# Kernel optimization log

Measured on AMD Instinct MI355X. Metric: run time of the kernel, lower is better.

The kernel has to match this reference:

```python
import jax, jax.numpy as jnp
import numpy as np

TOP_K = 2
NUM_EXPERTS = 8


def setup_inputs() -> dict:
    key = jax.random.key(0)
    ks = jax.random.split(key, 5)
    d_model, d_ff, E = 1024, 2048, NUM_EXPERTS
    B, S = 4, 1024
    scale = 1.0 / np.sqrt(d_model)
    return {
        "x": jax.random.normal(ks[0], (B, S, d_model), jnp.float32),
        "gate_w": jax.random.normal(ks[1], (E, d_model), jnp.float32) * scale,
        "w1": jax.random.normal(ks[2], (E, d_ff, d_model), jnp.float32) * scale,
        "w3": jax.random.normal(ks[3], (E, d_ff, d_model), jnp.float32) * scale,
        "w2": jax.random.normal(ks[4], (E, d_model, d_ff), jnp.float32) * (1.0 / np.sqrt(d_ff)),
    }


def reference(x, gate_w, w1, w3, w2):
    B, S, d = x.shape
    E = gate_w.shape[0]
    T = B * S

    # Router (eval mode: no noise)
    router_logits = jnp.einsum("bsd,ed->bse", x, gate_w)  # (B,S,E)
    top_logits, top_idx = jax.lax.top_k(router_logits, TOP_K)  # (B,S,k)
    routing_weights = jax.nn.softmax(top_logits, axis=-1)

    x_flat = x.reshape(T, d)
    idx_flat = top_idx.reshape(T, TOP_K)
    rw_flat = routing_weights.reshape(T, TOP_K)

    # (T,E) combine weights: topk indices are distinct, so one-hot sum is exact
    one_hot = jax.nn.one_hot(idx_flat, E, dtype=x.dtype)  # (T,k,E)
    combine = jnp.einsum("tke,tk->te", one_hot, rw_flat)  # (T,E)

    # Dense grouped SwiGLU: run every expert over all tokens, weight-combine.
    h = jnp.einsum("td,efd->tef", x_flat, w1)  # (T,E,d_ff)
    v = jnp.einsum("td,efd->tef", x_flat, w3)
    y = jax.nn.silu(h) * v
    expert_out = jnp.einsum("tef,edf->ted", y, w2)  # (T,E,d)
    out_flat = jnp.einsum("ted,te->td", expert_out, combine)
    output = out_flat.reshape(B, S, d)

    # Auxiliary load-balance loss
    router_probs = jax.nn.softmax(router_logits, axis=-1)  # (B,S,E)
    expert_probs = router_probs.mean(axis=(0, 1))  # (E,)
    counts = one_hot.sum(axis=(0, 1))  # (E,)
    expert_fraction = counts / (T * TOP_K)
    aux_loss = jnp.sum(expert_probs * expert_fraction) * E

    return output, aux_loss
```

## Files before the change

### kernel.cpp

```cpp
#include <hip/hip_runtime.h>
#include <hip/hip_bf16.h>
#include <stdint.h>

#define T_TOK 4096
#define DM    1024
#define DF    2048
#define NE    8
#define RROWS 8192
#define BM    128
#define BK    64
#define MAXT  72

typedef __attribute__((ext_vector_type(8))) short bf16x8;
typedef __attribute__((ext_vector_type(4))) float f32x4;

static __device__ __forceinline__ unsigned short f2bf(float f) {
  union { float f; unsigned u; } v; v.f = f;
  unsigned r = v.u + 0x7fffu + ((v.u >> 16) & 1u);
  return (unsigned short)(r >> 16);
}

static __device__ __forceinline__ void glds16(const void* g, void* l) {
  __builtin_amdgcn_global_load_lds(
      (__attribute__((address_space(1))) void*)(g),
      (__attribute__((address_space(3))) void*)(l), 16, 0, 0);
}

__global__ __launch_bounds__(256) void cvt_kernel(const float* __restrict__ src,
                                                  unsigned short* __restrict__ dst, int n4) {
  int stride = gridDim.x * blockDim.x;
  for (int i = blockIdx.x * blockDim.x + threadIdx.x; i < n4; i += stride) {
    float4 f = ((const float4*)src)[i];
    ushort4 u;
    u.x = f2bf(f.x); u.y = f2bf(f.y); u.z = f2bf(f.z); u.w = f2bf(f.w);
    ((ushort4*)dst)[i] = u;
  }
}

__global__ __launch_bounds__(256) void router_kernel(
    const float* __restrict__ x, const float* __restrict__ gw,
    unsigned short* __restrict__ xb,
    int* __restrict__ topk_idx, float* __restrict__ topk_w,
    int* __restrict__ pc, float* __restrict__ pp) {
  __shared__ int lc[8];
  __shared__ float lp[8];
  int wave = threadIdx.x >> 6;
  int lane = threadIdx.x & 63;
  if (threadIdx.x < 8) { lc[threadIdx.x] = 0; lp[threadIdx.x] = 0.f; }
  __syncthreads();

  int t = blockIdx.x * 4 + wave;

  const float4* xp = (const float4*)(x + (size_t)t * DM);
  float4 xv[4];
#pragma unroll
  for (int q = 0; q < 4; ++q) xv[q] = xp[lane + 64 * q];

  ushort4* xbp = (ushort4*)(xb + (size_t)t * DM);
#pragma unroll
  for (int q = 0; q < 4; ++q) {
    ushort4 u;
    u.x = f2bf(xv[q].x); u.y = f2bf(xv[q].y); u.z = f2bf(xv[q].z); u.w = f2bf(xv[q].w);
    xbp[lane + 64 * q] = u;
  }

  float l[NE];
#pragma unroll
  for (int e = 0; e < NE; ++e) {
    const float4* gp = (const float4*)(gw + (size_t)e * DM);
    float s = 0.f;
#pragma unroll
    for (int q = 0; q < 4; ++q) {
      float4 g4 = gp[lane + 64 * q];
      s += xv[q].x * g4.x + xv[q].y * g4.y + xv[q].z * g4.z + xv[q].w * g4.w;
    }
#pragma unroll
    for (int off = 32; off > 0; off >>= 1) s += __shfl_xor(s, off);
    l[e] = s;
  }

  float m = l[0];
#pragma unroll
  for (int e = 1; e < NE; ++e) m = fmaxf(m, l[e]);
  float p[NE], ps = 0.f;
#pragma unroll
  for (int e = 0; e < NE; ++e) { p[e] = expf(l[e] - m); ps += p[e]; }

  int i1 = 0; float v1 = l[0];
#pragma unroll
  for (int e = 1; e < NE; ++e) if (l[e] > v1) { v1 = l[e]; i1 = e; }
  int i2 = -1; float v2 = -1e30f;
#pragma unroll
  for (int e = 0; e < NE; ++e) if (e != i1 && l[e] > v2) { v2 = l[e]; i2 = e; }

  float r2 = expf(v2 - v1);
  float inv12 = 1.f / (1.f + r2);

  if (lane == 0) {
    topk_idx[t * 2] = i1; topk_idx[t * 2 + 1] = i2;
    topk_w[t * 2] = inv12; topk_w[t * 2 + 1] = r2 * inv12;
    atomicAdd(&lc[i1], 1);
    atomicAdd(&lc[i2], 1);
    float inv = 1.f / ps;
#pragma unroll
    for (int e = 0; e < NE; ++e) atomicAdd(&lp[e], p[e] * inv);
  }
  __syncthreads();
  if (threadIdx.x < 8) {
    pc[blockIdx.x * 8 + threadIdx.x] = lc[threadIdx.x];
    pp[blockIdx.x * 8 + threadIdx.x] = lp[threadIdx.x];
  }
}

__global__ __launch_bounds__(512) void reduce_aux_kernel(
    const int* __restrict__ pc, const float* __restrict__ pp,
    int* __restrict__ counts, float* __restrict__ out_aux) {
  __shared__ int sc[8];
  __shared__ float sp[8];
  int wave = threadIdx.x >> 6;
  int lane = threadIdx.x & 63;
  int c = 0; float p = 0.f;
#pragma unroll
  for (int j = 0; j < 16; ++j) {
    int idx = lane + 64 * j;
    c += pc[idx * 8 + wave];
    p += pp[idx * 8 + wave];
  }
#pragma unroll
  for (int off = 32; off > 0; off >>= 1) {
    c += __shfl_xor(c, off);
    p += __shfl_xor(p, off);
  }
  if (lane == 0) { sc[wave] = c; sp[wave] = p; counts[wave] = c; }
  __syncthreads();
  if (threadIdx.x == 0) {
    float s = 0.f;
#pragma unroll
    for (int e = 0; e < NE; ++e)
      s += (sp[e] / (float)T_TOK) * ((float)sc[e] / (float)(T_TOK * 2));
    *out_aux = s * (float)NE;
  }
}

__global__ void build_tiles_kernel(const int* __restrict__ counts, int* __restrict__ offsets,
                                   int* __restrict__ tiledesc, int* __restrict__ ntiles) {
  if (threadIdx.x != 0 || blockIdx.x != 0) return;
  int off = 0, nt = 0;
  for (int e = 0; e < NE; ++e) {
    offsets[e] = off;
    int n = counts[e];
    for (int r0 = 0; r0 < n; r0 += BM) {
      int rem = n - r0;
      tiledesc[nt * 3 + 0] = e;
      tiledesc[nt * 3 + 1] = off + r0;
      tiledesc[nt * 3 + 2] = rem < BM ? rem : BM;
      ++nt;
    }
    off += n;
  }
  offsets[NE] = off;
  *ntiles = nt;
}

__global__ __launch_bounds__(256) void scatter_kernel(
    const int* __restrict__ topk_idx, const float* __restrict__ topk_w,
    const int* __restrict__ offsets, int* __restrict__ fill,
    int* __restrict__ btok, float* __restrict__ bw) {
  __shared__ int lcnt[8], lbase[8];
  int i = blockIdx.x * 256 + threadIdx.x;
  if (threadIdx.x < 8) lcnt[threadIdx.x] = 0;
  __syncthreads();
  int e = topk_idx[i];
  int pos = atomicAdd(&lcnt[e], 1);
  __syncthreads();
  if (threadIdx.x < 8) lbase[threadIdx.x] = atomicAdd(&fill[threadIdx.x], lcnt[threadIdx.x]);
  __syncthreads();
  int j = offsets[e] + lbase[e] + pos;
  btok[j] = i >> 1;
  bw[j] = topk_w[i];
}

template <bool WB16>
__global__ __launch_bounds__(512) void gemm1_kernel(
    const unsigned short* __restrict__ xb,
    const void* __restrict__ w1p, const void* __restrict__ w3p,
    unsigned short* __restrict__ Y,
    const int* __restrict__ btok,
    const int* __restrict__ tiledesc, const int* __restrict__ ntiles) {
  int flat = blockIdx.y * MAXT + blockIdx.x;
  int total = MAXT * (DF / 128);
  int nid = (flat & 7) * (total >> 3) + (flat >> 3);
  int mt = nid % MAXT;
  int fb = nid / MAXT;

  if (mt >= *ntiles) return;
  int e    = tiledesc[mt * 3 + 0];
  int row0 = tiledesc[mt * 3 + 1];
  int mcnt = tiledesc[mt * 3 + 2];
  int f0   = fb * 128;

  __shared__ __align__(16) unsigned short sA[128 * 64];
  __shared__ __align__(16) unsigned short sB1[128 * 64];
  __shared__ __align__(16) unsigned short sB3[128 * 64];

  int tid = threadIdx.x;
  int w = tid >> 6, lane = tid & 63;
  int wm = w >> 2, wn = w & 3;

  int rA0 = w * 8 + (lane >> 3);
  int rA1 = rA0 + 64;
  int colb = (((lane & 7) ^ (lane >> 3)) << 4);
  int tok0 = btok[row0 + ((rA0 < mcnt) ? rA0 : 0)];
  int tok1 = btok[row0 + ((rA1 < mcnt) ? rA1 : 0)];

  const char* xbc = (const char*)xb;
  const char* w1c = (const char*)w1p;
  const char* w3c = (const char*)w3p;

  f32x4 acch[4][2] = {};
  f32x4 accv[4][2] = {};

  for (int k0 = 0; k0 < DM; k0 += BK) {
    __syncthreads();
    glds16(xbc + (((size_t)tok0 * DM + k0) * 2) + colb, (char*)sA + w * 1024);
    glds16(xbc + (((size_t)tok1 * DM + k0) * 2) + colb, (char*)sA + (w + 8) * 1024);
    if constexpr (WB16) {
      glds16(w1c + (((size_t)(e * DF + f0 + rA0) * DM + k0) * 2) + colb, (char*)sB1 + w * 1024);
      glds16(w1c + (((size_t)(e * DF + f0 + rA1) * DM + k0) * 2) + colb, (char*)sB1 + (w + 8) * 1024);
      glds16(w3c + (((size_t)(e * DF + f0 + rA0) * DM + k0) * 2) + colb, (char*)sB3 + w * 1024);
      glds16(w3c + (((size_t)(e * DF + f0 + rA1) * DM + k0) * 2) + colb, (char*)sB3 + (w + 8) * 1024);
    } else {
#pragma unroll
      for (int it = 0; it < 4; ++it) {
        int gidx = tid + it * 512;
        int r = gidx >> 4;
        int cb8 = (gidx & 15) * 8;
        int sw = cb8 ^ ((r & 7) << 4);
        size_t gbyte = (((size_t)(e * DF + f0 + r) * DM + k0) * 4) + (size_t)cb8 * 2;
        float4 f1 = *(const float4*)(w1c + gbyte);
        float4 f3 = *(const float4*)(w3c + gbyte);
        ushort4 u1, u3;
        u1.x = f2bf(f1.x); u1.y = f2bf(f1.y); u1.z = f2bf(f1.z); u1.w = f2bf(f1.w);
        u3.x = f2bf(f3.x); u3.y = f2bf(f3.y); u3.z = f2bf(f3.z); u3.w = f2bf(f3.w);
        *(ushort4*)((char*)sB1 + r * 128 + sw) = u1;
        *(ushort4*)((char*)sB3 + r * 128 + sw) = u3;
      }
    }
    __syncthreads();

#pragma unroll
    for (int kk = 0; kk < 2; ++kk) {
      int kb = ((lane >> 4) << 4) + kk * 64;
      bf16x8 a[4], b1f[2], b3f[2];
#pragma unroll
      for (int m = 0; m < 4; ++m) {
        int r = wm * 64 + m * 16 + (lane & 15);
        a[m] = *(const bf16x8*)((const char*)sA + r * 128 + (kb ^ ((r & 7) << 4)));
      }
#pragma unroll
      for (int n = 0; n < 2; ++n) {
        int rf = wn * 32 + n * 16 + (lane & 15);
        int ob = rf * 128 + (kb ^ ((rf & 7) << 4));
        b1f[n] = *(const bf16x8*)((const char*)sB1 + ob);
        b3f[n] = *(const bf16x8*)((const char*)sB3 + ob);
      }
#pragma unroll
      for (int m = 0; m < 4; ++m)
#pragma unroll
        for (int n = 0; n < 2; ++n) {
          acch[m][n] = __builtin_amdgcn_mfma_f32_16x16x32_bf16(a[m], b1f[n], acch[m][n], 0, 0, 0);
          accv[m][n] = __builtin_amdgcn_mfma_f32_16x16x32_bf16(a[m], b3f[n], accv[m][n], 0, 0, 0);
        }
    }
  }

#pragma unroll
  for (int m = 0; m < 4; ++m) {
#pragma unroll
    for (int j = 0; j < 4; ++j) {
      int rl = wm * 64 + m * 16 + (lane >> 4) * 4 + j;
      if (rl < mcnt) {
        size_t yrow = (size_t)(row0 + rl) * DF + f0;
#pragma unroll
        for (int n = 0; n < 2; ++n) {
          float h = acch[m][n][j], v = accv[m][n][j];
          float y = (h / (1.f + expf(-h))) * v;
          Y[yrow + wn * 32 + n * 16 + (lane & 15)] = f2bf(y);
        }
      }
    }
  }
}

template <bool WB16>
__global__ __launch_bounds__(512) void gemm2_kernel(
    const unsigned short* __restrict__ Y,
    const void* __restrict__ w2p,
    float* __restrict__ out,
    const int* __restrict__ btok, const float* __restrict__ bw,
    const int* __restrict__ tiledesc, const int* __restrict__ ntiles) {
  int flat = blockIdx.y * MAXT + blockIdx.x;
  int total = MAXT * (DM / 128);
  int nid = (flat & 7) * (total >> 3) + (flat >> 3);
  int mt = nid % MAXT;
  int cb = nid / MAXT;

  if (mt >= *ntiles) return;
  int e    = tiledesc[mt * 3 + 0];
  int row0 = tiledesc[mt * 3 + 1];
  int mcnt = tiledesc[mt * 3 + 2];
  int c0   = cb * 128;

  __shared__ __align__(16) unsigned short sA[128 * 64];
  __shared__ __align__(16) unsigned short sB[128 * 64];

  int tid = threadIdx.x;
  int w = tid >> 6, lane = tid & 63;
  int wm = w >> 2, wn = w & 3;

  int rA0 = w * 8 + (lane >> 3);
  int rA1 = rA0 + 64;
  int colb = (((lane & 7) ^ (lane >> 3)) << 4);

  const char* yc  = (const char*)Y;
  const char* w2c = (const char*)w2p;

  f32x4 acc[4][2] = {};

  for (int k0 = 0; k0 < DF; k0 += BK) {
    __syncthreads();
    glds16(yc + (((size_t)(row0 + rA0) * DF + k0) * 2) + colb, (char*)sA + w * 1024);
    glds16(yc + (((size_t)(row0 + rA1) * DF + k0) * 2) + colb, (char*)sA + (w + 8) * 1024);
    if constexpr (WB16) {
      glds16(w2c + (((size_t)(e * DM + c0 + rA0) * DF + k0) * 2) + colb, (char*)sB + w * 1024);
      glds16(w2c + (((size_t)(e * DM + c0 + rA1) * DF + k0) * 2) + colb, (char*)sB + (w + 8) * 1024);
    } else {
#pragma unroll
      for (int it = 0; it < 4; ++it) {
        int gidx = tid + it * 512;
        int r = gidx >> 4;
        int cb8 = (gidx & 15) * 8;
        int sw = cb8 ^ ((r & 7) << 4);
        size_t gbyte = (((size_t)(e * DM + c0 + r) * DF + k0) * 4) + (size_t)cb8 * 2;
        float4 f = *(const float4*)(w2c + gbyte);
        ushort4 u;
        u.x = f2bf(f.x); u.y = f2bf(f.y); u.z = f2bf(f.z); u.w = f2bf(f.w);
        *(ushort4*)((char*)sB + r * 128 + sw) = u;
      }
    }
    __syncthreads();

#pragma unroll
    for (int kk = 0; kk < 2; ++kk) {
      int kb = ((lane >> 4) << 4) + kk * 64;
      bf16x8 a[4], b[2];
#pragma unroll
      for (int m = 0; m < 4; ++m) {
        int r = wm * 64 + m * 16 + (lane & 15);
        a[m] = *(const bf16x8*)((const char*)sA + r * 128 + (kb ^ ((r & 7) << 4)));
      }
#pragma unroll
      for (int n = 0; n < 2; ++n) {
        int rf = wn * 32 + n * 16 + (lane & 15);
        b[n] = *(const bf16x8*)((const char*)sB + rf * 128 + (kb ^ ((rf & 7) << 4)));
      }
#pragma unroll
      for (int m = 0; m < 4; ++m)
#pragma unroll
        for (int n = 0; n < 2; ++n)
          acc[m][n] = __builtin_amdgcn_mfma_f32_16x16x32_bf16(a[m], b[n], acc[m][n], 0, 0, 0);
    }
  }

#pragma unroll
  for (int m = 0; m < 4; ++m) {
#pragma unroll
    for (int j = 0; j < 4; ++j) {
      int rl = wm * 64 + m * 16 + (lane >> 4) * 4 + j;
      if (rl < mcnt) {
        int tok = btok[row0 + rl];
        float wgt = bw[row0 + rl];
#pragma unroll
        for (int n = 0; n < 2; ++n) {
          int col = c0 + wn * 32 + n * 16 + (lane & 15);
          atomicAdd(&out[(size_t)tok * DM + col], wgt * acc[m][n][j]);
        }
      }
    }
  }
}

extern "C" void kernel_launch(void* const* d_in, const int* in_sizes, int n_in,
                              void* d_out, int out_size, void* d_ws, size_t ws_size,
                              hipStream_t stream) {
  const float* x  = (const float*)d_in[0];
  const float* gw = (const float*)d_in[1];
  const float* w1 = (const float*)d_in[2];
  const float* w3 = (const float*)d_in[3];
  const float* w2 = (const float*)d_in[4];
  float* out = (float*)d_out;

  char* ws = (char*)d_ws;
  size_t o = 0;
  auto alloc = [&](size_t b) { size_t r = o; o = (o + b + 255) & ~(size_t)255; return r; };
  size_t o_tidx = alloc((size_t)RROWS * 4);
  size_t o_tw   = alloc((size_t)RROWS * 4);
  size_t o_meta = alloc(4096);
  size_t o_desc = alloc((size_t)MAXT * 3 * 4);
  size_t o_btok = alloc((size_t)RROWS * 4);
  size_t o_bw   = alloc((size_t)RROWS * 4);
  size_t o_pc   = alloc((size_t)1024 * 8 * 4);
  size_t o_pp   = alloc((size_t)1024 * 8 * 4);
  size_t o_xb   = alloc((size_t)T_TOK * DM * 2);
  size_t o_Y    = alloc((size_t)(RROWS + 128) * DF * 2);
  size_t o_w1b  = alloc((size_t)NE * DF * DM * 2);
  size_t o_w3b  = alloc((size_t)NE * DF * DM * 2);
  size_t o_w2b  = alloc((size_t)NE * DM * DF * 2);
  size_t need_full = o;
  bool full = ws_size >= need_full;

  int* tidx   = (int*)(ws + o_tidx);
  float* tw   = (float*)(ws + o_tw);
  int* meta   = (int*)(ws + o_meta);
  int* counts = meta;
  int* fill   = meta + 8;
  int* offs   = meta + 16;
  int* ntiles = meta + 25;
  int* desc   = (int*)(ws + o_desc);
  int* btok   = (int*)(ws + o_btok);
  float* bw   = (float*)(ws + o_bw);
  int* pc     = (int*)(ws + o_pc);
  float* pp   = (float*)(ws + o_pp);
  unsigned short* xb = (unsigned short*)(ws + o_xb);
  unsigned short* Y  = (unsigned short*)(ws + o_Y);

  hipMemsetAsync(ws + o_meta, 0, 256, stream);
  hipMemsetAsync(d_out, 0, (size_t)T_TOK * DM * 4, stream);

  if (full) {
    cvt_kernel<<<2048, 256, 0, stream>>>(w1, (unsigned short*)(ws + o_w1b), NE * DF * DM / 4);
    cvt_kernel<<<2048, 256, 0, stream>>>(w3, (unsigned short*)(ws + o_w3b), NE * DF * DM / 4);
    cvt_kernel<<<2048, 256, 0, stream>>>(w2, (unsigned short*)(ws + o_w2b), NE * DM * DF / 4);
  }

  router_kernel<<<T_TOK / 4, 256, 0, stream>>>(x, gw, xb, tidx, tw, pc, pp);
  reduce_aux_kernel<<<1, 512, 0, stream>>>(pc, pp, counts, out + (size_t)T_TOK * DM);
  build_tiles_kernel<<<1, 1, 0, stream>>>(counts, offs, desc, ntiles);
  scatter_kernel<<<RROWS / 256, 256, 0, stream>>>(tidx, tw, offs, fill, btok, bw);

  if (full) {
    gemm1_kernel<true><<<dim3(MAXT, DF / 128), 512, 0, stream>>>(
        xb, ws + o_w1b, ws + o_w3b, Y, btok, desc, ntiles);
    gemm2_kernel<true><<<dim3(MAXT, DM / 128), 512, 0, stream>>>(
        Y, ws + o_w2b, out, btok, bw, desc, ntiles);
  } else {
    gemm1_kernel<false><<<dim3(MAXT, DF / 128), 512, 0, stream>>>(
        xb, w1, w3, Y, btok, desc, ntiles);
    gemm2_kernel<false><<<dim3(MAXT, DM / 128), 512, 0, stream>>>(
        Y, w2, out, btok, bw, desc, ntiles);
  }
}
```

Before: 264.6 us.

## Double M tile to 256, double-buffer LDS in expert GEMMs, merge weight casts

Both expert GEMMs now use 256-row token tiles (MAXT drops to 40), and each wave computes a 64x64 sub-tile instead of 64x32. This raises data reuse per shared-memory load and halves the redundant weight traffic across M tiles. The K loop is double-buffered: the next stage's async global-to-LDS loads are issued before the current stage's MFMAs, so memory latency overlaps compute. The three fp32→bf16 weight conversion launches are merged into one kernel with a 3-row grid. In exchange, LDS use and register pressure both rise, which likely limits occupancy to one block per CU.

After: 320.9 us. +21.3%, slower.

```diff
diff --git a/kernel.cpp b/kernel.cpp
--- a/kernel.cpp
+++ b/kernel.cpp
@@ -7,9 +7,9 @@
 #define DF    2048
 #define NE    8
 #define RROWS 8192
-#define BM    128
+#define BM    256
 #define BK    64
-#define MAXT  72
+#define MAXT  40
 
 typedef __attribute__((ext_vector_type(8))) short bf16x8;
 typedef __attribute__((ext_vector_type(4))) float f32x4;
@@ -26,8 +26,12 @@
       (__attribute__((address_space(3))) void*)(l), 16, 0, 0);
 }
 
-__global__ __launch_bounds__(256) void cvt_kernel(const float* __restrict__ src,
-                                                  unsigned short* __restrict__ dst, int n4) {
+__global__ __launch_bounds__(256) void cvt3_kernel(
+    const float* __restrict__ w1, const float* __restrict__ w3, const float* __restrict__ w2,
+    unsigned short* __restrict__ d1, unsigned short* __restrict__ d3, unsigned short* __restrict__ d2,
+    int n4) {
+  const float* src = blockIdx.y == 0 ? w1 : (blockIdx.y == 1 ? w3 : w2);
+  unsigned short* dst = blockIdx.y == 0 ? d1 : (blockIdx.y == 1 ? d3 : d2);
   int stride = gridDim.x * blockDim.x;
   for (int i = blockIdx.x * blockDim.x + threadIdx.x; i < n4; i += stride) {
     float4 f = ((const float4*)src)[i];
@@ -181,14 +185,14 @@
 }
 
 template <bool WB16>
-__global__ __launch_bounds__(512) void gemm1_kernel(
+__global__ __launch_bounds__(512, 2) void gemm1_kernel(
     const unsigned short* __restrict__ xb,
     const void* __restrict__ w1p, const void* __restrict__ w3p,
     unsigned short* __restrict__ Y,
     const int* __restrict__ btok,
     const int* __restrict__ tiledesc, const int* __restrict__ ntiles) {
   int flat = blockIdx.y * MAXT + blockIdx.x;
-  int total = MAXT * (DF / 128);
+  const int total = MAXT * (DF / 128);
   int nid = (flat & 7) * (total >> 3) + (flat >> 3);
   int mt = nid % MAXT;
   int fb = nid / MAXT;
@@ -199,36 +203,42 @@
   int mcnt = tiledesc[mt * 3 + 2];
   int f0   = fb * 128;
 
-  __shared__ __align__(16) unsigned short sA[128 * 64];
-  __shared__ __align__(16) unsigned short sB1[128 * 64];
-  __shared__ __align__(16) unsigned short sB3[128 * 64];
+  __shared__ __align__(16) unsigned short sA[2][BM * BK];
+  __shared__ __align__(16) unsigned short sB1[2][128 * BK];
+  __shared__ __align__(16) unsigned short sB3[2][128 * BK];
 
   int tid = threadIdx.x;
   int w = tid >> 6, lane = tid & 63;
-  int wm = w >> 2, wn = w & 3;
-
-  int rA0 = w * 8 + (lane >> 3);
-  int rA1 = rA0 + 64;
+  int wm = w >> 1, wn = w & 1;
   int colb = (((lane & 7) ^ (lane >> 3)) << 4);
-  int tok0 = btok[row0 + ((rA0 < mcnt) ? rA0 : 0)];
-  int tok1 = btok[row0 + ((rA1 < mcnt) ? rA1 : 0)];
+  int srow = w * 8 + (lane >> 3);
+
+  int tokr[4];
+#pragma unroll
+  for (int r = 0; r < 4; ++r) {
+    int row = r * 64 + srow;
+    tokr[r] = btok[row0 + ((row < mcnt) ? row : 0)];
+  }
 
   const char* xbc = (const char*)xb;
   const char* w1c = (const char*)w1p;
   const char* w3c = (const char*)w3p;
 
-  f32x4 acch[4][2] = {};
-  f32x4 accv[4][2] = {};
-
-  for (int k0 = 0; k0 < DM; k0 += BK) {
-    __syncthreads();
-    glds16(xbc + (((size_t)tok0 * DM + k0) * 2) + colb, (char*)sA + w * 1024);
-    glds16(xbc + (((size_t)tok1 * DM + k0) * 2) + colb, (char*)sA + (w + 8) * 1024);
+  f32x4 acch[4][4] = {};
+  f32x4 accv[4][4] = {};
+
+  auto stage = [&](int k0, int buf) {
+#pragma unroll
+    for (int r = 0; r < 4; ++r)
+      glds16(xbc + ((size_t)tokr[r] * DM + k0) * 2 + colb,
+             (char*)sA[buf] + r * 8192 + w * 1024);
     if constexpr (WB16) {
-      glds16(w1c + (((size_t)(e * DF + f0 + rA0) * DM + k0) * 2) + colb, (char*)sB1 + w * 1024);
-      glds16(w1c + (((size_t)(e * DF + f0 + rA1) * DM + k0) * 2) + colb, (char*)sB1 + (w + 8) * 1024);
-      glds16(w3c + (((size_t)(e * DF + f0 + rA0) * DM + k0) * 2) + colb, (char*)sB3 + w * 1024);
-      glds16(w3c + (((size_t)(e * DF + f0 + rA1) * DM + k0) * 2) + colb, (char*)sB3 + (w + 8) * 1024);
+#pragma unroll
+      for (int r = 0; r < 2; ++r) {
+        size_t broff = ((size_t)(e * DF + f0 + r * 64 + srow) * DM + k0) * 2;
+        glds16(w1c + broff + colb, (char*)sB1[buf] + r * 8192 + w * 1024);
+        glds16(w3c + broff + colb, (char*)sB3[buf] + r * 8192 + w * 1024);
+      }
     } else {
 #pragma unroll
       for (int it = 0; it < 4; ++it) {
@@ -236,42 +246,50 @@
         int r = gidx >> 4;
         int cb8 = (gidx & 15) * 8;
         int sw = cb8 ^ ((r & 7) << 4);
-        size_t gbyte = (((size_t)(e * DF + f0 + r) * DM + k0) * 4) + (size_t)cb8 * 2;
+        size_t gbyte = ((size_t)(e * DF + f0 + r) * DM + k0) * 4 + (size_t)cb8 * 2;
         float4 f1 = *(const float4*)(w1c + gbyte);
         float4 f3 = *(const float4*)(w3c + gbyte);
         ushort4 u1, u3;
         u1.x = f2bf(f1.x); u1.y = f2bf(f1.y); u1.z = f2bf(f1.z); u1.w = f2bf(f1.w);
         u3.x = f2bf(f3.x); u3.y = f2bf(f3.y); u3.z = f2bf(f3.z); u3.w = f2bf(f3.w);
-        *(ushort4*)((char*)sB1 + r * 128 + sw) = u1;
-        *(ushort4*)((char*)sB3 + r * 128 + sw) = u3;
-      }
-    }
-    __syncthreads();
-
+        *(ushort4*)((char*)sB1[buf] + r * 128 + sw) = u1;
+        *(ushort4*)((char*)sB3[buf] + r * 128 + sw) = u3;
+      }
+    }
+  };
+
+  stage(0, 0);
+  __syncthreads();
+  int cur = 0;
+  const int NT = DM / BK;
+  for (int t = 0; t < NT; ++t) {
+    if (t < NT - 1) stage((t + 1) * BK, cur ^ 1);
 #pragma unroll
     for (int kk = 0; kk < 2; ++kk) {
       int kb = ((lane >> 4) << 4) + kk * 64;
-      bf16x8 a[4], b1f[2], b3f[2];
+      bf16x8 a[4], b1[4], b3[4];
 #pragma unroll
       for (int m = 0; m < 4; ++m) {
         int r = wm * 64 + m * 16 + (lane & 15);
-        a[m] = *(const bf16x8*)((const char*)sA + r * 128 + (kb ^ ((r & 7) << 4)));
-      }
-#pragma unroll
-      for (int n = 0; n < 2; ++n) {
-        int rf = wn * 32 + n * 16 + (lane & 15);
+        a[m] = *(const bf16x8*)((const char*)sA[cur] + r * 128 + (kb ^ ((r & 7) << 4)));
+      }
+#pragma unroll
+      for (int n = 0; n < 4; ++n) {
+        int rf = wn * 64 + n * 16 + (lane & 15);
         int ob = rf * 128 + (kb ^ ((rf & 7) << 4));
-        b1f[n] = *(const bf16x8*)((const char*)sB1 + ob);
-        b3f[n] = *(const bf16x8*)((const char*)sB3 + ob);
+        b1[n] = *(const bf16x8*)((const char*)sB1[cur] + ob);
+        b3[n] = *(const bf16x8*)((const char*)sB3[cur] + ob);
       }
 #pragma unroll
       for (int m = 0; m < 4; ++m)
 #pragma unroll
-        for (int n = 0; n < 2; ++n) {
-          acch[m][n] = __builtin_amdgcn_mfma_f32_16x16x32_bf16(a[m], b1f[n], acch[m][n], 0, 0, 0);
-          accv[m][n] = __builtin_amdgcn_mfma_f32_16x16x32_bf16(a[m], b3f[n], accv[m][n], 0, 0, 0);
+        for (int n = 0; n < 4; ++n) {
+          acch[m][n] = __builtin_amdgcn_mfma_f32_16x16x32_bf16(a[m], b1[n], acch[m][n], 0, 0, 0);
+          accv[m][n] = __builtin_amdgcn_mfma_f32_16x16x32_bf16(a[m], b3[n], accv[m][n], 0, 0, 0);
         }
     }
+    __syncthreads();
+    cur ^= 1;
   }
 
 #pragma unroll
@@ -282,10 +300,10 @@
       if (rl < mcnt) {
         size_t yrow = (size_t)(row0 + rl) * DF + f0;
 #pragma unroll
-        for (int n = 0; n < 2; ++n) {
+        for (int n = 0; n < 4; ++n) {
           float h = acch[m][n][j], v = accv[m][n][j];
           float y = (h / (1.f + expf(-h))) * v;
-          Y[yrow + wn * 32 + n * 16 + (lane & 15)] = f2bf(y);
+          Y[yrow + wn * 64 + n * 16 + (lane & 15)] = f2bf(y);
         }
       }
     }
@@ -293,14 +311,14 @@
 }
 
 template <bool WB16>
-__global__ __launch_bounds__(512) void gemm2_kernel(
+__global__ __launch_bounds__(512, 2) void gemm2_kernel(
     const unsigned short* __restrict__ Y,
     const void* __restrict__ w2p,
     float* __restrict__ out,
     const int* __restrict__ btok, const float* __restrict__ bw,
     const int* __restrict__ tiledesc, const int* __restrict__ ntiles) {
   int flat = blockIdx.y * MAXT + blockIdx.x;
-  int total = MAXT * (DM / 128);
+  const int total = MAXT * (DM / 128);
   int nid = (flat & 7) * (total >> 3) + (flat >> 3);
   int mt = nid % MAXT;
   int cb = nid / MAXT;
@@ -311,29 +329,31 @@
   int mcnt = tiledesc[mt * 3 + 2];
   int c0   = cb * 128;
 
-  __shared__ __align__(16) unsigned short sA[128 * 64];
-  __shared__ __align__(16) unsigned short sB[128 * 64];
+  __shared__ __align__(16) unsigned short sA[2][BM * BK];
+  __shared__ __align__(16) unsigned short sB[2][128 * BK];
 
   int tid = threadIdx.x;
   int w = tid >> 6, lane = tid & 63;
-  int wm = w >> 2, wn = w & 3;
-
-  int rA0 = w * 8 + (lane >> 3);
-  int rA1 = rA0 + 64;
+  int wm = w >> 1, wn = w & 1;
   int colb = (((lane & 7) ^ (lane >> 3)) << 4);
+  int srow = w * 8 + (lane >> 3);
 
   const char* yc  = (const char*)Y;
   const char* w2c = (const char*)w2p;
 
-  f32x4 acc[4][2] = {};
-
-  for (int k0 = 0; k0 < DF; k0 += BK) {
-    __syncthreads();
-    glds16(yc + (((size_t)(row0 + rA0) * DF + k0) * 2) + colb, (char*)sA + w * 1024);
-    glds16(yc + (((size_t)(row0 + rA1) * DF + k0) * 2) + colb, (char*)sA + (w + 8) * 1024);
+  f32x4 acc[4][4] = {};
+
+  auto stage = [&](int k0, int buf) {
+#pragma unroll
+    for (int r = 0; r < 4; ++r)
+      glds16(yc + ((size_t)(row0 + r * 64 + srow) * DF + k0) * 2 + colb,
+             (char*)sA[buf] + r * 8192 + w * 1024);
     if constexpr (WB16) {
-      glds16(w2c + (((size_t)(e * DM + c0 + rA0) * DF + k0) * 2) + colb, (char*)sB + w * 1024);
-      glds16(w2c + (((size_t)(e * DM + c0 + rA1) * DF + k0) * 2) + colb, (char*)sB + (w + 8) * 1024);
+#pragma unroll
+      for (int r = 0; r < 2; ++r) {
+        size_t broff = ((size_t)(e * DM + c0 + r * 64 + srow) * DF + k0) * 2;
+        glds16(w2c + broff + colb, (char*)sB[buf] + r * 8192 + w * 1024);
+      }
     } else {
 #pragma unroll
       for (int it = 0; it < 4; ++it) {
@@ -341,35 +361,43 @@
         int r = gidx >> 4;
         int cb8 = (gidx & 15) * 8;
         int sw = cb8 ^ ((r & 7) << 4);
-        size_t gbyte = (((size_t)(e * DM + c0 + r) * DF + k0) * 4) + (size_t)cb8 * 2;
+        size_t gbyte = ((size_t)(e * DM + c0 + r) * DF + k0) * 4 + (size_t)cb8 * 2;
         float4 f = *(const float4*)(w2c + gbyte);
         ushort4 u;
         u.x = f2bf(f.x); u.y = f2bf(f.y); u.z = f2bf(f.z); u.w = f2bf(f.w);
-        *(ushort4*)((char*)sB + r * 128 + sw) = u;
-      }
-    }
-    __syncthreads();
-
+        *(ushort4*)((char*)sB[buf] + r * 128 + sw) = u;
+      }
+    }
+  };
+
+  stage(0, 0);
+  __syncthreads();
+  int cur = 0;
+  const int NT = DF / BK;
+  for (int t = 0; t < NT; ++t) {
+    if (t < NT - 1) stage((t + 1) * BK, cur ^ 1);
 #pragma unroll
     for (int kk = 0; kk < 2; ++kk) {
       int kb = ((lane >> 4) << 4) + kk * 64;
-      bf16x8 a[4], b[2];
+      bf16x8 a[4], b[4];
 #pragma unroll
       for (int m = 0; m < 4; ++m) {
         int r = wm * 64 + m * 16 + (lane & 15);
-        a[m] = *(const bf16x8*)((const char*)sA + r * 128 + (kb ^ ((r & 7) << 4)));
-      }
-#pragma unroll
-      for (int n = 0; n < 2; ++n) {
-        int rf = wn * 32 + n * 16 + (lane & 15);
-        b[n] = *(const bf16x8*)((const char*)sB + rf * 128 + (kb ^ ((rf & 7) << 4)));
+        a[m] = *(const bf16x8*)((const char*)sA[cur] + r * 128 + (kb ^ ((r & 7) << 4)));
+      }
+#pragma unroll
+      for (int n = 0; n < 4; ++n) {
+        int rf = wn * 64 + n * 16 + (lane & 15);
+        b[n] = *(const bf16x8*)((const char*)sB[cur] + rf * 128 + (kb ^ ((rf & 7) << 4)));
       }
 #pragma unroll
       for (int m = 0; m < 4; ++m)
 #pragma unroll
-        for (int n = 0; n < 2; ++n)
+        for (int n = 0; n < 4; ++n)
           acc[m][n] = __builtin_amdgcn_mfma_f32_16x16x32_bf16(a[m], b[n], acc[m][n], 0, 0, 0);
     }
+    __syncthreads();
+    cur ^= 1;
   }
 
 #pragma unroll
@@ -381,8 +409,8 @@
         int tok = btok[row0 + rl];
         float wgt = bw[row0 + rl];
 #pragma unroll
-        for (int n = 0; n < 2; ++n) {
-          int col = c0 + wn * 32 + n * 16 + (lane & 15);
+        for (int n = 0; n < 4; ++n) {
+          int col = c0 + wn * 64 + n * 16 + (lane & 15);
           atomicAdd(&out[(size_t)tok * DM + col], wgt * acc[m][n][j]);
         }
       }
@@ -412,7 +440,7 @@
   size_t o_pc   = alloc((size_t)1024 * 8 * 4);
   size_t o_pp   = alloc((size_t)1024 * 8 * 4);
   size_t o_xb   = alloc((size_t)T_TOK * DM * 2);
-  size_t o_Y    = alloc((size_t)(RROWS + 128) * DF * 2);
+  size_t o_Y    = alloc((size_t)(RROWS + 256) * DF * 2);
   size_t o_w1b  = alloc((size_t)NE * DF * DM * 2);
   size_t o_w3b  = alloc((size_t)NE * DF * DM * 2);
   size_t o_w2b  = alloc((size_t)NE * DM * DF * 2);
@@ -438,9 +466,10 @@
   hipMemsetAsync(d_out, 0, (size_t)T_TOK * DM * 4, stream);
 
   if (full) {
-    cvt_kernel<<<2048, 256, 0, stream>>>(w1, (unsigned short*)(ws + o_w1b), NE * DF * DM / 4);
-    cvt_kernel<<<2048, 256, 0, stream>>>(w3, (unsigned short*)(ws + o_w3b), NE * DF * DM / 4);
-    cvt_kernel<<<2048, 256, 0, stream>>>(w2, (unsigned short*)(ws + o_w2b), NE * DM * DF / 4);
+    cvt3_kernel<<<dim3(2048, 3), 256, 0, stream>>>(
+        w1, w3, w2,
+        (unsigned short*)(ws + o_w1b), (unsigned short*)(ws + o_w3b),
+        (unsigned short*)(ws + o_w2b), NE * DF * DM / 4);
   }
 
   router_kernel<<<T_TOK / 4, 256, 0, stream>>>(x, gw, xb, tidx, tw, pc, pp);
```

## Rewrite gate/up GEMM with 256-row tiles, double-buffered LDS and phased MFMA schedule

Applied to the files above, without the earlier changes.

Replaces the first grouped GEMM with a kernel that uses 256-row token tiles (a separate tile descriptor list), double-buffered shared memory, and an 8-phase schedule. The schedule interleaves async global-to-LDS prefetch of the next K step with MFMA clusters, using explicit vmcnt waits, barriers and setprio. The three weight-conversion launches are also merged into one 2D-grid kernel. Larger tiles raise weight reuse and the prefetch hides load latency. The cost is more registers and LDS per block, plus more padding waste on partial expert tiles.

Measured after the change: 273.3 us. 1.03x slower.

```diff
diff --git a/kernel.cpp b/kernel.cpp
--- a/kernel.cpp
+++ b/kernel.cpp
@@ -7,9 +7,9 @@
 #define DF    2048
 #define NE    8
 #define RROWS 8192
-#define BM    128
 #define BK    64
-#define MAXT  72
+#define MAXT1 40
+#define MAXT2 72
 
 typedef __attribute__((ext_vector_type(8))) short bf16x8;
 typedef __attribute__((ext_vector_type(4))) float f32x4;
@@ -26,8 +26,18 @@
       (__attribute__((address_space(3))) void*)(l), 16, 0, 0);
 }
 
-__global__ __launch_bounds__(256) void cvt_kernel(const float* __restrict__ src,
-                                                  unsigned short* __restrict__ dst, int n4) {
+#define VM_WAIT2 do { asm volatile("s_waitcnt vmcnt(2)" ::: "memory"); \
+                      __builtin_amdgcn_sched_barrier(0); } while (0)
+#define VM_WAIT0 do { asm volatile("s_waitcnt vmcnt(0)" ::: "memory"); \
+                      __builtin_amdgcn_sched_barrier(0); } while (0)
+#define BARRIER __builtin_amdgcn_s_barrier()
+
+__global__ __launch_bounds__(256) void cvt3_kernel(
+    const float* __restrict__ w1, const float* __restrict__ w3, const float* __restrict__ w2,
+    unsigned short* __restrict__ d1, unsigned short* __restrict__ d3, unsigned short* __restrict__ d2,
+    int n4) {
+  const float* src = blockIdx.y == 0 ? w1 : (blockIdx.y == 1 ? w3 : w2);
+  unsigned short* dst = blockIdx.y == 0 ? d1 : (blockIdx.y == 1 ? d3 : d2);
   int stride = gridDim.x * blockDim.x;
   for (int i = blockIdx.x * blockDim.x + threadIdx.x; i < n4; i += stride) {
     float4 f = ((const float4*)src)[i];
@@ -143,23 +153,28 @@
 }
 
 __global__ void build_tiles_kernel(const int* __restrict__ counts, int* __restrict__ offsets,
-                                   int* __restrict__ tiledesc, int* __restrict__ ntiles) {
+                                   int* __restrict__ d1, int* __restrict__ nt1p,
+                                   int* __restrict__ d2, int* __restrict__ nt2p) {
   if (threadIdx.x != 0 || blockIdx.x != 0) return;
-  int off = 0, nt = 0;
+  int off = 0, nt1 = 0, nt2 = 0;
   for (int e = 0; e < NE; ++e) {
     offsets[e] = off;
     int n = counts[e];
-    for (int r0 = 0; r0 < n; r0 += BM) {
+    for (int r0 = 0; r0 < n; r0 += 256) {
       int rem = n - r0;
-      tiledesc[nt * 3 + 0] = e;
-      tiledesc[nt * 3 + 1] = off + r0;
-      tiledesc[nt * 3 + 2] = rem < BM ? rem : BM;
-      ++nt;
+      d1[nt1 * 3 + 0] = e; d1[nt1 * 3 + 1] = off + r0; d1[nt1 * 3 + 2] = rem < 256 ? rem : 256;
+      ++nt1;
+    }
+    for (int r0 = 0; r0 < n; r0 += 128) {
+      int rem = n - r0;
+      d2[nt2 * 3 + 0] = e; d2[nt2 * 3 + 1] = off + r0; d2[nt2 * 3 + 2] = rem < 128 ? rem : 128;
+      ++nt2;
     }
     off += n;
   }
   offsets[NE] = off;
-  *ntiles = nt;
+  *nt1p = nt1;
+  *nt2p = nt2;
 }
 
 __global__ __launch_bounds__(256) void scatter_kernel(
@@ -180,19 +195,180 @@
   bw[j] = topk_w[i];
 }
 
-template <bool WB16>
-__global__ __launch_bounds__(512) void gemm1_kernel(
+__global__ __launch_bounds__(512, 2) void gemm1_8p(
     const unsigned short* __restrict__ xb,
-    const void* __restrict__ w1p, const void* __restrict__ w3p,
+    const unsigned short* __restrict__ w1b, const unsigned short* __restrict__ w3b,
+    unsigned short* __restrict__ Y,
+    const int* __restrict__ btok,
+    const int* __restrict__ desc1, const int* __restrict__ ntiles1) {
+  int flat = blockIdx.y * MAXT1 + blockIdx.x;
+  const int total = MAXT1 * (DF / 128);
+  int nid = (flat & 7) * (total >> 3) + (flat >> 3);
+  int mt = nid % MAXT1;
+  int fb = nid / MAXT1;
+  if (mt >= *ntiles1) return;
+  int e    = desc1[mt * 3 + 0];
+  int row0 = desc1[mt * 3 + 1];
+  int mcnt = desc1[mt * 3 + 2];
+  int f0   = fb * 128;
+
+  __shared__ __align__(16) unsigned short sA[2][256 * 64];
+  __shared__ __align__(16) unsigned short sB1[2][128 * 64];
+  __shared__ __align__(16) unsigned short sB3[2][128 * 64];
+
+  int tid = threadIdx.x;
+  int w = tid >> 6, lane = tid & 63;
+  int wm = w >> 2, wn = w & 3;
+  int sr = w * 8 + (lane >> 3);
+  int colb = ((lane & 7) ^ (lane >> 3)) << 4;
+  int kbase = (lane >> 4) * 16;
+
+  int tokr[4];
+#pragma unroll
+  for (int u = 0; u < 4; ++u) {
+    int row = u * 64 + sr;
+    tokr[u] = btok[row0 + ((row < mcnt) ? row : 0)];
+  }
+
+  const char* xc  = (const char*)xb;
+  const char* w1c = (const char*)w1b;
+  const char* w3c = (const char*)w3b;
+
+  f32x4 acch[8][2] = {};
+  f32x4 accv[8][2] = {};
+
+  auto stA = [&](int u, int k0, int b) {
+    glds16(xc + ((size_t)tokr[u] * DM + k0) * 2 + colb,
+           (char*)sA[b] + u * 8192 + w * 1024);
+  };
+  auto stB = [&](const char* wsrc, unsigned short* dst, int u, int k0) {
+    glds16(wsrc + ((size_t)(e * DF + f0 + u * 64 + sr) * DM + k0) * 2 + colb,
+           (char*)dst + u * 8192 + w * 1024);
+  };
+
+  stA(0, 0, 0); stA(1, 0, 0); stA(2, 0, 0); stA(3, 0, 0);
+  stB(w1c, sB1[0], 0, 0); stB(w1c, sB1[0], 1, 0);
+  stB(w3c, sB3[0], 0, 0); stB(w3c, sB3[0], 1, 0);
+  VM_WAIT2;
+  BARRIER;
+
+  const int NT = DM / BK;
+  int cur = 0;
+  for (int t = 0; t < NT; ++t) {
+    bool pre = (t + 1 < NT);
+    int k1 = (t + 1) * BK;
+    bf16x8 a0[8], a1[8], bf[2];
+
+#pragma unroll
+    for (int m = 0; m < 8; ++m) {
+      int r = wm * 128 + m * 16 + (lane & 15);
+      a0[m] = *(const bf16x8*)((const char*)sA[cur] + r * 128 + (kbase ^ ((r & 7) << 4)));
+    }
+#pragma unroll
+    for (int n = 0; n < 2; ++n) {
+      int r = n * 64 + wn * 16 + (lane & 15);
+      bf[n] = *(const bf16x8*)((const char*)sB1[cur] + r * 128 + (kbase ^ ((r & 7) << 4)));
+    }
+    if (pre) { stA(0, k1, cur ^ 1); stA(1, k1, cur ^ 1); VM_WAIT2; }
+    else VM_WAIT0;
+    BARRIER;
+    __builtin_amdgcn_s_setprio(1);
+#pragma unroll
+    for (int m = 0; m < 8; ++m)
+#pragma unroll
+      for (int n = 0; n < 2; ++n)
+        acch[m][n] = __builtin_amdgcn_mfma_f32_16x16x32_bf16(a0[m], bf[n], acch[m][n], 0, 0, 0);
+    __builtin_amdgcn_s_setprio(0);
+    BARRIER;
+
+#pragma unroll
+    for (int n = 0; n < 2; ++n) {
+      int r = n * 64 + wn * 16 + (lane & 15);
+      bf[n] = *(const bf16x8*)((const char*)sB3[cur] + r * 128 + (kbase ^ ((r & 7) << 4)));
+    }
+    if (pre) { stA(2, k1, cur ^ 1); stA(3, k1, cur ^ 1); }
+    BARRIER;
+    __builtin_amdgcn_s_setprio(1);
+#pragma unroll
+    for (int m = 0; m < 8; ++m)
+#pragma unroll
+      for (int n = 0; n < 2; ++n)
+        accv[m][n] = __builtin_amdgcn_mfma_f32_16x16x32_bf16(a0[m], bf[n], accv[m][n], 0, 0, 0);
+    __builtin_amdgcn_s_setprio(0);
+    BARRIER;
+
+#pragma unroll
+    for (int m = 0; m < 8; ++m) {
+      int r = wm * 128 + m * 16 + (lane & 15);
+      a1[m] = *(const bf16x8*)((const char*)sA[cur] + r * 128 + ((kbase + 64) ^ ((r & 7) << 4)));
+    }
+#pragma unroll
+    for (int n = 0; n < 2; ++n) {
+      int r = n * 64 + wn * 16 + (lane & 15);
+      bf[n] = *(const bf16x8*)((const char*)sB1[cur] + r * 128 + ((kbase + 64) ^ ((r & 7) << 4)));
+    }
+    if (pre) { stB(w1c, sB1[cur ^ 1], 0, k1); stB(w1c, sB1[cur ^ 1], 1, k1); }
+    BARRIER;
+    __builtin_amdgcn_s_setprio(1);
+#pragma unroll
+    for (int m = 0; m < 8; ++m)
+#pragma unroll
+      for (int n = 0; n < 2; ++n)
+        acch[m][n] = __builtin_amdgcn_mfma_f32_16x16x32_bf16(a1[m], bf[n], acch[m][n], 0, 0, 0);
+    __builtin_amdgcn_s_setprio(0);
+    BARRIER;
+
+#pragma unroll
+    for (int n = 0; n < 2; ++n) {
+      int r = n * 64 + wn * 16 + (lane & 15);
+      bf[n] = *(const bf16x8*)((const char*)sB3[cur] + r * 128 + ((kbase + 64) ^ ((r & 7) << 4)));
+    }
+    if (pre) {
+      stB(w3c, sB3[cur ^ 1], 0, k1); stB(w3c, sB3[cur ^ 1], 1, k1);
+      VM_WAIT2;
+    }
+    BARRIER;
+    __builtin_amdgcn_s_setprio(1);
+#pragma unroll
+    for (int m = 0; m < 8; ++m)
+#pragma unroll
+      for (int n = 0; n < 2; ++n)
+        accv[m][n] = __builtin_amdgcn_mfma_f32_16x16x32_bf16(a1[m], bf[n], accv[m][n], 0, 0, 0);
+    __builtin_amdgcn_s_setprio(0);
+    BARRIER;
+
+    cur ^= 1;
+  }
+
+#pragma unroll
+  for (int m = 0; m < 8; ++m) {
+#pragma unroll
+    for (int j = 0; j < 4; ++j) {
+      int rl = wm * 128 + m * 16 + (lane >> 4) * 4 + j;
+      if (rl < mcnt) {
+        size_t yrow = (size_t)(row0 + rl) * DF + f0;
+#pragma unroll
+        for (int n = 0; n < 2; ++n) {
+          float h = acch[m][n][j], v = accv[m][n][j];
+          float y = (h / (1.f + expf(-h))) * v;
+          Y[yrow + n * 64 + wn * 16 + (lane & 15)] = f2bf(y);
+        }
+      }
+    }
+  }
+}
+
+__global__ __launch_bounds__(512) void gemm1_fb(
+    const unsigned short* __restrict__ xb,
+    const float* __restrict__ w1p, const float* __restrict__ w3p,
     unsigned short* __restrict__ Y,
     const int* __restrict__ btok,
     const int* __restrict__ tiledesc, const int* __restrict__ ntiles) {
-  int flat = blockIdx.y * MAXT + blockIdx.x;
-  int total = MAXT * (DF / 128);
+  int flat = blockIdx.y * MAXT2 + blockIdx.x;
+  const int total = MAXT2 * (DF / 128);
   int nid = (flat & 7) * (total >> 3) + (flat >> 3);
-  int mt = nid % MAXT;
-  int fb = nid / MAXT;
-
+  int mt = nid % MAXT2;
+  int fb = nid / MAXT2;
   if (mt >= *ntiles) return;
   int e    = tiledesc[mt * 3 + 0];
   int row0 = tiledesc[mt * 3 + 1];
@@ -206,7 +382,6 @@
   int tid = threadIdx.x;
   int w = tid >> 6, lane = tid & 63;
   int wm = w >> 2, wn = w & 3;
-
   int rA0 = w * 8 + (lane >> 3);
   int rA1 = rA0 + 64;
   int colb = (((lane & 7) ^ (lane >> 3)) << 4);
@@ -224,30 +399,22 @@
     __syncthreads();
     glds16(xbc + (((size_t)tok0 * DM + k0) * 2) + colb, (char*)sA + w * 1024);
     glds16(xbc + (((size_t)tok1 * DM + k0) * 2) + colb, (char*)sA + (w + 8) * 1024);
-    if constexpr (WB16) {
-      glds16(w1c + (((size_t)(e * DF + f0 + rA0) * DM + k0) * 2) + colb, (char*)sB1 + w * 1024);
-      glds16(w1c + (((size_t)(e * DF + f0 + rA1) * DM + k0) * 2) + colb, (char*)sB1 + (w + 8) * 1024);
-      glds16(w3c + (((size_t)(e * DF + f0 + rA0) * DM + k0) * 2) + colb, (char*)sB3 + w * 1024);
-      glds16(w3c + (((size_t)(e * DF + f0 + rA1) * DM + k0) * 2) + colb, (char*)sB3 + (w + 8) * 1024);
-    } else {
-#pragma unroll
-      for (int it = 0; it < 4; ++it) {
-        int gidx = tid + it * 512;
-        int r = gidx >> 4;
-        int cb8 = (gidx & 15) * 8;
-        int sw = cb8 ^ ((r & 7) << 4);
-        size_t gbyte = (((size_t)(e * DF + f0 + r) * DM + k0) * 4) + (size_t)cb8 * 2;
-        float4 f1 = *(const float4*)(w1c + gbyte);
-        float4 f3 = *(const float4*)(w3c + gbyte);
-        ushort4 u1, u3;
-        u1.x = f2bf(f1.x); u1.y = f2bf(f1.y); u1.z = f2bf(f1.z); u1.w = f2bf(f1.w);
-        u3.x = f2bf(f3.x); u3.y = f2bf(f3.y); u3.z = f2bf(f3.z); u3.w = f2bf(f3.w);
-        *(ushort4*)((char*)sB1 + r * 128 + sw) = u1;
-        *(ushort4*)((char*)sB3 + r * 128 + sw) = u3;
-      }
+#pragma unroll
+    for (int it = 0; it < 4; ++it) {
+      int gidx = tid + it * 512;
+      int r = gidx >> 4;
+      int cb8 = (gidx & 15) * 8;
+      int sw = cb8 ^ ((r & 7) << 4);
+      size_t gbyte = (((size_t)(e * DF + f0 + r) * DM + k0) * 4) + (size_t)cb8 * 2;
+      float4 f1 = *(const float4*)(w1c + gbyte);
+      float4 f3 = *(const float4*)(w3c + gbyte);
+      ushort4 u1, u3;
+      u1.x = f2bf(f1.x); u1.y = f2bf(f1.y); u1.z = f2bf(f1.z); u1.w = f2bf(f1.w);
+      u3.x = f2bf(f3.x); u3.y = f2bf(f3.y); u3.z = f2bf(f3.z); u3.w = f2bf(f3.w);
+      *(ushort4*)((char*)sB1 + r * 128 + sw) = u1;
+      *(ushort4*)((char*)sB3 + r * 128 + sw) = u3;
     }
     __syncthreads();
-
 #pragma unroll
     for (int kk = 0; kk < 2; ++kk) {
       int kb = ((lane >> 4) << 4) + kk * 64;
@@ -273,7 +440,6 @@
         }
     }
   }
-
 #pragma unroll
   for (int m = 0; m < 4; ++m) {
 #pragma unroll
@@ -299,12 +465,11 @@
     float* __restrict__ out,
     const int* __restrict__ btok, const float* __restrict__ bw,
     const int* __restrict__ tiledesc, const int* __restrict__ ntiles) {
-  int flat = blockIdx.y * MAXT + blockIdx.x;
-  int total = MAXT * (DM / 128);
+  int flat = blockIdx.y * MAXT2 + blockIdx.x;
+  const int total = MAXT2 * (DM / 128);
   int nid = (flat & 7) * (total >> 3) + (flat >> 3);
-  int mt = nid % MAXT;
-  int cb = nid / MAXT;
-
+  int mt = nid % MAXT2;
+  int cb = nid / MAXT2;
   if (mt >= *ntiles) return;
   int e    = tiledesc[mt * 3 + 0];
   int row0 = tiledesc[mt * 3 + 1];
@@ -317,7 +482,6 @@
   int tid = threadIdx.x;
   int w = tid >> 6, lane = tid & 63;
   int wm = w >> 2, wn = w & 3;
-
   int rA0 = w * 8 + (lane >> 3);
   int rA1 = rA0 + 64;
   int colb = (((lane & 7) ^ (lane >> 3)) << 4);
@@ -349,7 +513,6 @@
       }
     }
     __syncthreads();
-
 #pragma unroll
     for (int kk = 0; kk < 2; ++kk) {
       int kb = ((lane >> 4) << 4) + kk * 64;
@@ -406,13 +569,14 @@
   size_t o_tidx = alloc((size_t)RROWS * 4);
   size_t o_tw   = alloc((size_t)RROWS * 4);
   size_t o_meta = alloc(4096);
-  size_t o_desc = alloc((size_t)MAXT * 3 * 4);
+  size_t o_d1   = alloc((size_t)MAXT1 * 3 * 4);
+  size_t o_d2   = alloc((size_t)MAXT2 * 3 * 4);
   size_t o_btok = alloc((size_t)RROWS * 4);
   size_t o_bw   = alloc((size_t)RROWS * 4);
   size_t o_pc   = alloc((size_t)1024 * 8 * 4);
   size_t o_pp   = alloc((size_t)1024 * 8 * 4);
   size_t o_xb   = alloc((size_t)T_TOK * DM * 2);
-  size_t o_Y    = alloc((size_t)(RROWS + 128) * DF * 2);
+  size_t o_Y    = alloc((size_t)(RROWS + 256) * DF * 2);
   size_t o_w1b  = alloc((size_t)NE * DF * DM * 2);
   size_t o_w3b  = alloc((size_t)NE * DF * DM * 2);
   size_t o_w2b  = alloc((size_t)NE * DM * DF * 2);
@@ -425,8 +589,10 @@
   int* counts = meta;
   int* fill   = meta + 8;
   int* offs   = meta + 16;
-  int* ntiles = meta + 25;
-  int* desc   = (int*)(ws + o_desc);
+  int* nt1    = meta + 25;
+  int* nt2    = meta + 26;
+  int* d1     = (int*)(ws + o_d1);
+  int* d2     = (int*)(ws + o_d2);
   int* btok   = (int*)(ws + o_btok);
   float* bw   = (float*)(ws + o_bw);
   int* pc     = (int*)(ws + o_pc);
@@ -438,25 +604,27 @@
   hipMemsetAsync(d_out, 0, (size_t)T_TOK * DM * 4, stream);
 
   if (full) {
-    cvt_kernel<<<2048, 256, 0, stream>>>(w1, (unsigned short*)(ws + o_w1b), NE * DF * DM / 4);
-    cvt_kernel<<<2048, 256, 0, stream>>>(w3, (unsigned short*)(ws + o_w3b), NE * DF * DM / 4);
-    cvt_kernel<<<2048, 256, 0, stream>>>(w2, (unsigned short*)(ws + o_w2b), NE * DM * DF / 4);
+    cvt3_kernel<<<dim3(2048, 3), 256, 0, stream>>>(
+        w1, w3, w2,
+        (unsigned short*)(ws + o_w1b), (unsigned short*)(ws + o_w3b),
+        (unsigned short*)(ws + o_w2b), NE * DF * DM / 4);
   }
 
   router_kernel<<<T_TOK / 4, 256, 0, stream>>>(x, gw, xb, tidx, tw, pc, pp);
   reduce_aux_kernel<<<1, 512, 0, stream>>>(pc, pp, counts, out + (size_t)T_TOK * DM);
-  build_tiles_kernel<<<1, 1, 0, stream>>>(counts, offs, desc, ntiles);
+  build_tiles_kernel<<<1, 1, 0, stream>>>(counts, offs, d1, nt1, d2, nt2);
   scatter_kernel<<<RROWS / 256, 256, 0, stream>>>(tidx, tw, offs, fill, btok, bw);
 
   if (full) {
-    gemm1_kernel<true><<<dim3(MAXT, DF / 128), 512, 0, stream>>>(
-        xb, ws + o_w1b, ws + o_w3b, Y, btok, desc, ntiles);
-    gemm2_kernel<true><<<dim3(MAXT, DM / 128), 512, 0, stream>>>(
-        Y, ws + o_w2b, out, btok, bw, desc, ntiles);
+    gemm1_8p<<<dim3(MAXT1, DF / 128), 512, 0, stream>>>(
+        xb, (const unsigned short*)(ws + o_w1b), (const unsigned short*)(ws + o_w3b),
+        Y, btok, d1, nt1);
+    gemm2_kernel<true><<<dim3(MAXT2, DM / 128), 512, 0, stream>>>(
+        Y, ws + o_w2b, out, btok, bw, d2, nt2);
   } else {
-    gemm1_kernel<false><<<dim3(MAXT, DF / 128), 512, 0, stream>>>(
-        xb, w1, w3, Y, btok, desc, ntiles);
-    gemm2_kernel<false><<<dim3(MAXT, DM / 128), 512, 0, stream>>>(
-        Y, w2, out, btok, bw, desc, ntiles);
-  }
-}
+    gemm1_fb<<<dim3(MAXT2, DF / 128), 512, 0, stream>>>(
+        xb, w1, w3, Y, btok, d2, nt2);
+    gemm2_kernel<false><<<dim3(MAXT2, DM / 128), 512, 0, stream>>>(
+        Y, w2, out, btok, bw, d2, nt2);
+  }
+}
```
